# Performance work log

Measured on AMD Instinct MI355X. Metric: run time of the kernel, lower is better.

## Reference

```python
import jax, jax.numpy as jnp
import numpy as np

MODEL_DIM = 2048
N_HEADS = 16
T_MAX = 2048
LATENT = 512
DHR = 64
DK = MODEL_DIM // N_HEADS  # 128
B = 4
T = 2048


def _rope_tables(t, d):
    # pos pattern [0,0,1,1,...] matching repeat(2).reshape in source
    pos = jnp.repeat(jnp.arange(d // 2, dtype=jnp.float32), 2)
    theta = jnp.power(10000.0, -2.0 * pos / d)  # (d,)
    freq = jnp.arange(t, dtype=jnp.float32)[:, None]  # (t,1)
    ang = freq * theta[None, :]  # (t,d)
    return jnp.cos(ang), jnp.sin(ang)


def _apply_rope(x, cos, sin):
    # x: (B, nh, T, d); interleaved rotate-half: (x1,x2) -> (-x2, x1)
    b, nh, t, d = x.shape
    x2 = x.reshape(b, nh, t, d // 2, 2)
    x_rot = jnp.stack([-x2[..., 1], x2[..., 0]], axis=-1).reshape(b, nh, t, d)
    return x * cos[None, None] + x_rot * sin[None, None]


def setup_inputs() -> dict:
    key = jax.random.key(0)
    ks = jax.random.split(key, 14)
    s = 0.02
    f32 = jnp.float32
    return {
        "x": jax.random.normal(ks[0], (B, T, MODEL_DIM), dtype=f32),
        "W_down": jax.random.normal(ks[1], (MODEL_DIM, 2 * LATENT), dtype=f32) * s,
        "b_down": jnp.zeros((2 * LATENT,), dtype=f32),
        "W_uKV": jax.random.normal(ks[2], (LATENT, 2 * MODEL_DIM), dtype=f32) * s,
        "b_uKV": jnp.zeros((2 * MODEL_DIM,), dtype=f32),
        "W_uQ": jax.random.normal(ks[3], (LATENT, MODEL_DIM), dtype=f32) * s,
        "b_uQ": jnp.zeros((MODEL_DIM,), dtype=f32),
        "W_kr": jax.random.normal(ks[4], (MODEL_DIM, DHR), dtype=f32) * s,
        "b_kr": jnp.zeros((DHR,), dtype=f32),
        "W_qr": jax.random.normal(ks[5], (MODEL_DIM, DHR * N_HEADS), dtype=f32) * s,
        "b_qr": jnp.zeros((DHR * N_HEADS,), dtype=f32),
        "W_out": jax.random.normal(ks[6], (MODEL_DIM, MODEL_DIM), dtype=f32) * s,
        "b_out": jnp.zeros((MODEL_DIM,), dtype=f32),
    }


def reference(x, W_down, b_down, W_uKV, b_uKV, W_uQ, b_uQ,
              W_kr, b_kr, W_qr, b_qr, W_out, b_out):
    b, t, c = x.shape
    cos, sin = _rope_tables(T_MAX, DHR)
    cos, sin = cos[:t], sin[:t]

    # low-rank down projection -> latent for KV and latent for Q
    down = x @ W_down + b_down  # (B,T,2*LATENT)
    cKV, cq = jnp.split(down, 2, axis=-1)

    # decoupled RoPE channels
    kR = _apply_rope((x @ W_kr + b_kr)[:, None], cos, sin)  # (B,1,T,dhR)
    kR = jnp.broadcast_to(kR, (b, N_HEADS, t, DHR))
    qR = (x @ W_qr + b_qr).reshape(b, t, N_HEADS, DHR).transpose(0, 2, 1, 3)
    qR = _apply_rope(qR, cos, sin)  # (B,nh,T,dhR)

    # up-projections
    v_k = (cKV @ W_uKV + b_uKV).reshape(b, t, N_HEADS, 2 * DK).transpose(0, 2, 1, 3)
    v, k = jnp.split(v_k, 2, axis=-1)  # (B,nh,T,dk) each
    k = jnp.concatenate([k, kR], axis=-1)  # (B,nh,T,dk+dhR)
    q = (cq @ W_uQ + b_uQ).reshape(b, t, N_HEADS, DK).transpose(0, 2, 1, 3)
    q = jnp.concatenate([q, qR], axis=-1)  # (B,nh,T,dk+dhR)

    # scaled dot-product attention (unmasked, as in source; scale uses dk only)
    w = jnp.einsum('bhtd,bhsd->bhts', q, k) * (1.0 / DK ** 0.5)
    w = jax.nn.softmax(w, axis=-1)
    out = jnp.einsum('bhts,bhsd->bhtd', w, v)  # (B,nh,T,dk)
    out = out.transpose(0, 2, 1, 3).reshape(b, t, MODEL_DIM)
    return out @ W_out + b_out
```

## Files before the change

kernel.cpp:

```cpp
#include <hip/hip_runtime.h>
#include <hip/hip_bf16.h>

typedef unsigned short u16;
typedef unsigned int u32;
typedef __attribute__((ext_vector_type(4))) float f32x4;
typedef __attribute__((ext_vector_type(8))) short s16x8;

#define NHEADS 16
#define TSEQ 2048
#define BATCH 4
#define BT (BATCH*TSEQ)

__device__ __forceinline__ float bf2f(u16 v){ u32 u=((u32)v)<<16; return __builtin_bit_cast(float,u); }
__device__ __forceinline__ u16 f2bf(float f){ u32 u=__builtin_bit_cast(u32,f); u += 0x7fffu + ((u>>16)&1u); return (u16)(u>>16); }

__device__ __forceinline__ void gload16(const void* g, void* l){
  __builtin_amdgcn_global_load_lds((const __attribute__((address_space(1))) u32*)g,
                                   (__attribute__((address_space(3))) u32*)l, 16, 0, 0);
}

__global__ void cast_bf16_kernel(const float* __restrict__ in, u16* __restrict__ out, long n){
  long i = ((long)blockIdx.x*256 + threadIdx.x)*4;
  if (i >= n) return;
  float4 v = *(const float4*)(in + i);
  ushort4 o;
  o.x = f2bf(v.x); o.y = f2bf(v.y); o.z = f2bf(v.z); o.w = f2bf(v.w);
  *(ushort4*)(out + i) = o;
}

__global__ void transpose_cast_kernel(const float* __restrict__ in, u16* __restrict__ out, int R, int C){
  __shared__ float tile[32][33];
  int bc = blockIdx.x*32, br = blockIdx.y*32;
  int lx = threadIdx.x & 31, ly = threadIdx.x >> 5;
  #pragma unroll
  for (int i=0;i<32;i+=8)
    tile[ly+i][lx] = in[(long)(br+ly+i)*C + bc + lx];
  __syncthreads();
  #pragma unroll
  for (int i=0;i<32;i+=8)
    out[(long)(bc+ly+i)*R + br + lx] = f2bf(tile[lx][ly+i]);
}

__global__ void rope_tab_kernel(float* __restrict__ ctab, float* __restrict__ stab){
  int idx = blockIdx.x*256 + threadIdx.x;
  int t = idx >> 5, i = idx & 31;
  float theta = expf(-(float)i * (9.210340371976184f/32.0f));
  float ang = (float)t * theta;
  float s, c;
  sincosf(ang, &s, &c);
  ctab[idx] = c; stab[idx] = s;
}

__global__ void rope_inplace_kernel(u32* __restrict__ buf, const float* __restrict__ ct,
                                    const float* __restrict__ st, int log2ppr){
  long idx = (long)blockIdx.x*256 + threadIdx.x;
  long row = idx >> log2ppr;
  int pp = (int)(idx & ((1<<log2ppr)-1));
  int t = (int)(row & (TSEQ-1));
  int pr = pp & 31;
  u32 v = buf[idx];
  float x0 = bf2f((u16)v), x1 = bf2f((u16)(v>>16));
  float c = ct[t*32+pr], s = st[t*32+pr];
  float y0 = x0*c - x1*s;
  float y1 = x1*c + x0*s;
  buf[idx] = (u32)f2bf(y0) | ((u32)f2bf(y1)<<16);
}

template<int OUTF32>
__global__ __launch_bounds__(256,2) void gemm_bt_kernel(
    const u16* __restrict__ A, const u16* __restrict__ Bt, const float* __restrict__ bias,
    void* __restrict__ Cp, int M, int N, int K, int lda, int ldb, int ldc)
{
  __shared__ u16 As[128*32];
  __shared__ u16 Bs[128*32];
  const int tid = threadIdx.x;
  const int lane = tid & 63;
  const int wave = tid >> 6;
  const long bm = (long)blockIdx.x * 128;
  const long bn = (long)blockIdx.y * 128;
  const int wr = (wave>>1)*64, wc = (wave&1)*64;
  const int g = lane>>4, r15 = lane&15;

  f32x4 acc[4][4];
  #pragma unroll
  for (int m=0;m<4;m++)
    #pragma unroll
    for (int n=0;n<4;n++) acc[m][n] = (f32x4){0.f,0.f,0.f,0.f};

  const int c0 = tid, c1 = tid + 256;
  const u16* gA0 = A + (bm + (c0>>2))*lda + (c0&3)*8;
  const u16* gA1 = A + (bm + (c1>>2))*lda + (c1&3)*8;
  const u16* gB0 = Bt + (bn + (c0>>2))*ldb + (c0&3)*8;
  const u16* gB1 = Bt + (bn + (c1>>2))*ldb + (c1&3)*8;
  u16* lA0 = As + c0*8;
  u16* lA1 = As + c1*8;
  u16* lB0 = Bs + c0*8;
  u16* lB1 = Bs + c1*8;

  for (int k0 = 0; k0 < K; k0 += 32) {
    __syncthreads();
    gload16(gA0 + k0, lA0);
    gload16(gA1 + k0, lA1);
    gload16(gB0 + k0, lB0);
    gload16(gB1 + k0, lB1);
    __syncthreads();
    s16x8 af[4], bfr[4];
    #pragma unroll
    for (int m=0;m<4;m++) af[m] = *(const s16x8*)(As + (wr + m*16 + r15)*32 + g*8);
    #pragma unroll
    for (int n=0;n<4;n++) bfr[n] = *(const s16x8*)(Bs + (wc + n*16 + r15)*32 + g*8);
    #pragma unroll
    for (int m=0;m<4;m++)
      #pragma unroll
      for (int n=0;n<4;n++)
        acc[m][n] = __builtin_amdgcn_mfma_f32_16x16x32_bf16(af[m], bfr[n], acc[m][n], 0,0,0);
  }

  #pragma unroll
  for (int n=0;n<4;n++){
    long col = bn + wc + n*16 + r15;
    if (col >= N) continue;
    float bv = bias[col];
    #pragma unroll
    for (int m=0;m<4;m++){
      long row0 = bm + wr + m*16 + g*4;
      #pragma unroll
      for (int i=0;i<4;i++){
        long row = row0 + i;
        if (row < M){
          float v = acc[m][n][i] + bv;
          if (OUTF32) ((float*)Cp)[row*(long)ldc + col] = v;
          else        ((u16*)Cp)[row*(long)ldc + col] = f2bf(v);
        }
      }
    }
  }
}

__global__ void transpose_v_kernel(const u16* __restrict__ vk_b, u16* __restrict__ Vt){
  __shared__ u16 tile[128][130];
  int t0 = blockIdx.x*128;
  int bh = blockIdx.y;
  int b = bh>>4, h = bh&15;
  for (int idx = threadIdx.x; idx < 128*128; idx += 256){
    int r = idx>>7, c = idx&127;
    tile[r][c] = vk_b[((long)(b*TSEQ + t0 + r))*4096 + h*256 + c];
  }
  __syncthreads();
  for (int idx = threadIdx.x; idx < 128*128; idx += 256){
    int d = idx>>7, tt = idx&127;
    Vt[((long)bh*128 + d)*TSEQ + t0 + tt] = tile[tt][d];
  }
}

__global__ __launch_bounds__(256,2) void attn_kernel(
    const u16* __restrict__ q_b, const u16* __restrict__ qr_b,
    const u16* __restrict__ vk_b, const u16* __restrict__ kr_b,
    const u16* __restrict__ Vt, u16* __restrict__ attn_b)
{
  __shared__ u16 Ks[64*192];
  __shared__ u16 Vs[128*64];
  __shared__ u16 Ps[4][16*64];

  const int tid = threadIdx.x;
  const int lane = tid & 63;
  const int wave = tid >> 6;
  const int g = lane >> 4;
  const int r15 = lane & 15;
  const int bh = blockIdx.y;
  const int b = bh>>4, h = bh&15;
  const int q0 = blockIdx.x*64 + wave*16;

  s16x8 qf[6];
  {
    const u16* qp  = q_b  + ((long)b*TSEQ + q0 + r15)*2048 + h*128 + g*8;
    const u16* qrp = qr_b + ((long)b*TSEQ + q0 + r15)*1024 + h*64  + g*8;
    #pragma unroll
    for (int kd=0;kd<4;kd++) qf[kd] = *(const s16x8*)(qp + kd*32);
    #pragma unroll
    for (int kd=4;kd<6;kd++) qf[kd] = *(const s16x8*)(qrp + (kd-4)*32);
  }

  f32x4 oacc[8];
  #pragma unroll
  for (int i=0;i<8;i++) oacc[i] = (f32x4){0.f,0.f,0.f,0.f};
  float mrow[4] = {-__builtin_inff(),-__builtin_inff(),-__builtin_inff(),-__builtin_inff()};
  float lrow[4] = {0.f,0.f,0.f,0.f};

  const int krow_s = tid>>2;
  const int kslot_s = tid&3;
  const int vrow_s = tid>>1;
  const int vslot_s = tid&1;
  const u16* kbase = vk_b + (long)b*TSEQ*4096 + h*256 + 128 + kslot_s*8;
  const u16* rbase = kr_b + (long)b*TSEQ*64 + kslot_s*8;
  const long vg_base = (long)bh*128*TSEQ;
  char* KsB = (char*)Ks;
  char* VsB = (char*)Vs;
  char* PsB = (char*)(&Ps[wave][0]);

  for (int kt=0; kt<32; ++kt) {
    __syncthreads();
    {
      long t = (long)(kt*64 + krow_s);
      u32 base = (u32)((krow_s*24 + kslot_s)*16);
      u32 sw = (u32)((krow_s&7)<<4);
      #pragma unroll
      for (int j=0;j<4;j++){
        s16x8 v = *(const s16x8*)(kbase + t*4096 + j*32);
        *(s16x8*)(KsB + ((base + j*64) ^ sw)) = v;
      }
      #pragma unroll
      for (int j=4;j<6;j++){
        s16x8 v = *(const s16x8*)(rbase + t*64 + (j-4)*32);
        *(s16x8*)(KsB + ((base + j*64) ^ sw)) = v;
      }
      const u16* vsrc = Vt + vg_base + (long)vrow_s*TSEQ + kt*64 + vslot_s*8;
      u32 vbase = (u32)((vrow_s*8 + vslot_s)*16);
      u32 vsw = (u32)((vrow_s&7)<<4);
      #pragma unroll
      for (int j=0;j<4;j++){
        s16x8 v = *(const s16x8*)(vsrc + j*16);
        *(s16x8*)(VsB + ((vbase + j*32) ^ vsw)) = v;
      }
    }
    __syncthreads();

    f32x4 sacc[4];
    #pragma unroll
    for (int n=0;n<4;n++) sacc[n] = (f32x4){0.f,0.f,0.f,0.f};
    #pragma unroll
    for (int kd=0; kd<6; kd++){
      #pragma unroll
      for (int n=0;n<4;n++){
        int krow = n*16 + r15;
        u32 byt = (u32)(krow*384 + kd*64 + g*16) ^ (u32)((krow&7)<<4);
        s16x8 kfr = *(const s16x8*)(KsB + byt);
        sacc[n] = __builtin_amdgcn_mfma_f32_16x16x32_bf16(qf[kd], kfr, sacc[n], 0,0,0);
      }
    }

    const float scale = 0.08838834764831845f;
    float tmax[4];
    #pragma unroll
    for (int i=0;i<4;i++){
      float m0 = fmaxf(fmaxf(sacc[0][i],sacc[1][i]), fmaxf(sacc[2][i],sacc[3][i]));
      #pragma unroll
      for (int off=1; off<16; off<<=1) m0 = fmaxf(m0, __shfl_xor(m0, off));
      tmax[i] = m0*scale;
    }
    float psc[4];
    #pragma unroll
    for (int i=0;i<4;i++){
      float mn = fmaxf(mrow[i], tmax[i]);
      psc[i] = __expf(mrow[i]-mn);
      mrow[i] = mn;
    }
    float rs[4] = {0.f,0.f,0.f,0.f};
    #pragma unroll
    for (int n=0;n<4;n++){
      #pragma unroll
      for (int i=0;i<4;i++){
        float p = __expf(sacc[n][i]*scale - mrow[i]);
        rs[i] += p;
        int prow = g*4+i;
        u32 pb = (u32)(prow*128 + (n*16+r15)*2) ^ (u32)((prow&7)<<4);
        *(u16*)(PsB + pb) = f2bf(p);
      }
    }
    #pragma unroll
    for (int i=0;i<4;i++){
      float rsum = rs[i];
      #pragma unroll
      for (int off=1; off<16; off<<=1) rsum += __shfl_xor(rsum, off);
      lrow[i] = lrow[i]*psc[i] + rsum;
    }
    #pragma unroll
    for (int nf=0;nf<8;nf++){
      f32x4 o = oacc[nf];
      o[0]*=psc[0]; o[1]*=psc[1]; o[2]*=psc[2]; o[3]*=psc[3];
      oacc[nf] = o;
    }
    #pragma unroll
    for (int ks=0; ks<2; ks++){
      u32 pb = (u32)(r15*128 + ks*64 + g*16) ^ (u32)((r15&7)<<4);
      s16x8 pf = *(const s16x8*)(PsB + pb);
      #pragma unroll
      for (int nf=0;nf<8;nf++){
        int vrow = nf*16 + r15;
        u32 vb = (u32)(vrow*128 + ks*64 + g*16) ^ (u32)((vrow&7)<<4);
        s16x8 vf = *(const s16x8*)(VsB + vb);
        oacc[nf] = __builtin_amdgcn_mfma_f32_16x16x32_bf16(pf, vf, oacc[nf], 0,0,0);
      }
    }
  }

  #pragma unroll
  for (int nf=0;nf<8;nf++){
    #pragma unroll
    for (int i=0;i<4;i++){
      float v = oacc[nf][i] / lrow[i];
      long t = q0 + g*4 + i;
      attn_b[((long)b*TSEQ + t)*2048 + h*128 + nf*16 + r15] = f2bf(v);
    }
  }
}

extern "C" void kernel_launch(void* const* d_in, const int* in_sizes, int n_in,
                              void* d_out, int out_size, void* d_ws, size_t ws_size,
                              hipStream_t stream)
{
  const float* x      = (const float*)d_in[0];
  const float* W_down = (const float*)d_in[1];
  const float* b_down = (const float*)d_in[2];
  const float* W_uKV  = (const float*)d_in[3];
  const float* b_uKV  = (const float*)d_in[4];
  const float* W_uQ   = (const float*)d_in[5];
  const float* b_uQ   = (const float*)d_in[6];
  const float* W_kr   = (const float*)d_in[7];
  const float* b_kr   = (const float*)d_in[8];
  const float* W_qr   = (const float*)d_in[9];
  const float* b_qr   = (const float*)d_in[10];
  const float* W_out  = (const float*)d_in[11];
  const float* b_out  = (const float*)d_in[12];
  float* out = (float*)d_out;

  char* ws = (char*)d_ws;
  size_t off = 0;
  auto alloc = [&](size_t b)->char* { char* p = ws + off; off += (b + 255) & ~(size_t)255; return p; };

  u16* xb     = (u16*)alloc((size_t)BT*2048*2);
  u16* attn_b = xb;
  u16* q_b    = (u16*)alloc((size_t)BT*2048*2);
  u16* vk_b   = (u16*)alloc((size_t)BT*4096*2);
  u16* qr_b   = (u16*)alloc((size_t)BT*1024*2);
  u16* kr_b   = (u16*)alloc((size_t)BT*64*2);
  char* slot5 = alloc((size_t)64*128*TSEQ*2);
  u16* down_b = (u16*)slot5;
  u16* Vt     = (u16*)slot5;
  u16* Wd_t   = (u16*)alloc((size_t)1024*2048*2);
  u16* Wqr_t  = (u16*)alloc((size_t)1024*2048*2);
  u16* Wkr_t  = (u16*)alloc((size_t)128*2048*2);
  u16* WuKV_t = (u16*)alloc((size_t)4096*512*2);
  u16* WuQ_t  = (u16*)alloc((size_t)2048*512*2);
  u16* Wout_t = (u16*)alloc((size_t)2048*2048*2);
  float* ctab = (float*)alloc((size_t)2048*32*4);
  float* stab = (float*)alloc((size_t)2048*32*4);

  long nx = (long)BT*2048;
  cast_bf16_kernel<<<dim3((u32)(nx/4/256)), 256, 0, stream>>>(x, xb, nx);
  transpose_cast_kernel<<<dim3(32, 64), 256, 0, stream>>>(W_down, Wd_t, 2048, 1024);
  transpose_cast_kernel<<<dim3(32, 64), 256, 0, stream>>>(W_qr,  Wqr_t, 2048, 1024);
  transpose_cast_kernel<<<dim3(2, 64),  256, 0, stream>>>(W_kr,  Wkr_t, 2048, 64);
  transpose_cast_kernel<<<dim3(128,16), 256, 0, stream>>>(W_uKV, WuKV_t, 512, 4096);
  transpose_cast_kernel<<<dim3(64, 16), 256, 0, stream>>>(W_uQ,  WuQ_t, 512, 2048);
  transpose_cast_kernel<<<dim3(64, 64), 256, 0, stream>>>(W_out, Wout_t, 2048, 2048);
  rope_tab_kernel<<<dim3(256), 256, 0, stream>>>(ctab, stab);

  gemm_bt_kernel<0><<<dim3(64, 8),  256, 0, stream>>>(xb, Wd_t,  b_down, down_b, 8192, 1024, 2048, 2048, 2048, 1024);
  gemm_bt_kernel<0><<<dim3(64, 8),  256, 0, stream>>>(xb, Wqr_t, b_qr,   qr_b,   8192, 1024, 2048, 2048, 2048, 1024);
  gemm_bt_kernel<0><<<dim3(64, 1),  256, 0, stream>>>(xb, Wkr_t, b_kr,   kr_b,   8192, 64,   2048, 2048, 2048, 64);
  gemm_bt_kernel<0><<<dim3(64, 32), 256, 0, stream>>>(down_b,       WuKV_t, b_uKV, vk_b, 8192, 4096, 512, 1024, 512, 4096);
  gemm_bt_kernel<0><<<dim3(64, 16), 256, 0, stream>>>(down_b + 512, WuQ_t,  b_uQ,  q_b,  8192, 2048, 512, 1024, 512, 2048);

  rope_inplace_kernel<<<dim3(16384), 256, 0, stream>>>((u32*)qr_b, ctab, stab, 9);
  rope_inplace_kernel<<<dim3(1024),  256, 0, stream>>>((u32*)kr_b, ctab, stab, 5);
  transpose_v_kernel<<<dim3(16, 64), 256, 0, stream>>>(vk_b, Vt);

  attn_kernel<<<dim3(32, 64), 256, 0, stream>>>(q_b, qr_b, vk_b, kr_b, Vt, attn_b);

  gemm_bt_kernel<1><<<dim3(64, 16), 256, 0, stream>>>(attn_b, Wout_t, b_out, out, 8192, 2048, 2048, 2048, 2048, 2048);
}
```

Measured before the change: 927.0 us.

## Fuse input projections into one GEMM, prefetch attention tiles, add lazy rescale

Concatenates W_down, W_qr and W_kr into a single transposed weight, so the three x-projections run as one wider GEMM with a concatenated bias. The rope kernels and attention read strided slices of that buffer, and Vt now lives in the output buffer as scratch. The attention kernel prefetches the next K/V tile into registers while computing, raises wave priority around the MFMA blocks, and skips the online-softmax rescale unless the running max grows by more than 8. The lazy rescale risks fp32 overflow or precision loss, and the register prefetch raises register pressure.

```diff
diff --git a/kernel.cpp b/kernel.cpp
--- a/kernel.cpp
+++ b/kernel.cpp
@@ -51,19 +51,31 @@
   ctab[idx] = c; stab[idx] = s;
 }
 
+__global__ void concat_bias_kernel(const float* __restrict__ a, const float* __restrict__ b,
+                                   const float* __restrict__ c, float* __restrict__ o){
+  int i = blockIdx.x*256 + threadIdx.x;
+  if (i >= 2176) return;
+  float v = 0.f;
+  if (i < 1024) v = a[i];
+  else if (i < 2048) v = b[i-1024];
+  else if (i < 2112) v = c[i-2048];
+  o[i] = v;
+}
+
 __global__ void rope_inplace_kernel(u32* __restrict__ buf, const float* __restrict__ ct,
-                                    const float* __restrict__ st, int log2ppr){
+                                    const float* __restrict__ st, int log2ppr, int rstride){
   long idx = (long)blockIdx.x*256 + threadIdx.x;
   long row = idx >> log2ppr;
   int pp = (int)(idx & ((1<<log2ppr)-1));
   int t = (int)(row & (TSEQ-1));
   int pr = pp & 31;
-  u32 v = buf[idx];
+  u32* p = buf + row*(long)rstride + pp;
+  u32 v = *p;
   float x0 = bf2f((u16)v), x1 = bf2f((u16)(v>>16));
   float c = ct[t*32+pr], s = st[t*32+pr];
   float y0 = x0*c - x1*s;
   float y1 = x1*c + x0*s;
-  buf[idx] = (u32)f2bf(y0) | ((u32)f2bf(y1)<<16);
+  *p = (u32)f2bf(y0) | ((u32)f2bf(y1)<<16);
 }
 
 template<int OUTF32>
@@ -154,8 +166,8 @@
 }
 
 __global__ __launch_bounds__(256,2) void attn_kernel(
-    const u16* __restrict__ q_b, const u16* __restrict__ qr_b,
-    const u16* __restrict__ vk_b, const u16* __restrict__ kr_b,
+    const u16* __restrict__ q_b, const u16* __restrict__ qrB,
+    const u16* __restrict__ vk_b, const u16* __restrict__ krB,
     const u16* __restrict__ Vt, u16* __restrict__ attn_b)
 {
   __shared__ u16 Ks[64*192];
@@ -173,12 +185,12 @@
 
   s16x8 qf[6];
   {
-    const u16* qp  = q_b  + ((long)b*TSEQ + q0 + r15)*2048 + h*128 + g*8;
-    const u16* qrp = qr_b + ((long)b*TSEQ + q0 + r15)*1024 + h*64  + g*8;
+    const u16* qp  = q_b + ((long)b*TSEQ + q0 + r15)*2048 + h*128 + g*8;
+    const u16* qrp = qrB + ((long)b*TSEQ + q0 + r15)*2112 + h*64  + g*8;
     #pragma unroll
     for (int kd=0;kd<4;kd++) qf[kd] = *(const s16x8*)(qp + kd*32);
-    #pragma unroll
-    for (int kd=4;kd<6;kd++) qf[kd] = *(const s16x8*)(qrp + (kd-4)*32);
+    qf[4] = *(const s16x8*)(qrp);
+    qf[5] = *(const s16x8*)(qrp + 32);
   }
 
   f32x4 oacc[8];
@@ -192,42 +204,50 @@
   const int vrow_s = tid>>1;
   const int vslot_s = tid&1;
   const u16* kbase = vk_b + (long)b*TSEQ*4096 + h*256 + 128 + kslot_s*8;
-  const u16* rbase = kr_b + (long)b*TSEQ*64 + kslot_s*8;
+  const u16* rbase = krB + (long)b*TSEQ*2112 + kslot_s*8;
   const long vg_base = (long)bh*128*TSEQ;
   char* KsB = (char*)Ks;
   char* VsB = (char*)Vs;
   char* PsB = (char*)(&Ps[wave][0]);
 
+  s16x8 kreg[6], vreg[4];
+
+  auto load_regs = [&](int kt){
+    long t = (long)(kt*64 + krow_s);
+    const u16* kp = kbase + t*4096;
+    const u16* rp = rbase + t*2112;
+    #pragma unroll
+    for (int j=0;j<4;j++) kreg[j] = *(const s16x8*)(kp + j*32);
+    kreg[4] = *(const s16x8*)(rp);
+    kreg[5] = *(const s16x8*)(rp + 32);
+    const u16* vsrc = Vt + vg_base + (long)vrow_s*TSEQ + kt*64 + vslot_s*8;
+    #pragma unroll
+    for (int j=0;j<4;j++) vreg[j] = *(const s16x8*)(vsrc + j*16);
+  };
+  auto write_lds = [&](){
+    u32 base = (u32)((krow_s*24 + kslot_s)*16);
+    u32 sw = (u32)((krow_s&7)<<4);
+    #pragma unroll
+    for (int j=0;j<6;j++)
+      *(s16x8*)(KsB + ((base + j*64) ^ sw)) = kreg[j];
+    u32 vbase = (u32)((vrow_s*8 + vslot_s)*16);
+    u32 vsw = (u32)((vrow_s&7)<<4);
+    #pragma unroll
+    for (int j=0;j<4;j++)
+      *(s16x8*)(VsB + ((vbase + j*32) ^ vsw)) = vreg[j];
+  };
+
+  load_regs(0);
+  write_lds();
+  __syncthreads();
+
   for (int kt=0; kt<32; ++kt) {
-    __syncthreads();
-    {
-      long t = (long)(kt*64 + krow_s);
-      u32 base = (u32)((krow_s*24 + kslot_s)*16);
-      u32 sw = (u32)((krow_s&7)<<4);
-      #pragma unroll
-      for (int j=0;j<4;j++){
-        s16x8 v = *(const s16x8*)(kbase + t*4096 + j*32);
-        *(s16x8*)(KsB + ((base + j*64) ^ sw)) = v;
-      }
-      #pragma unroll
-      for (int j=4;j<6;j++){
-        s16x8 v = *(const s16x8*)(rbase + t*64 + (j-4)*32);
-        *(s16x8*)(KsB + ((base + j*64) ^ sw)) = v;
-      }
-      const u16* vsrc = Vt + vg_base + (long)vrow_s*TSEQ + kt*64 + vslot_s*8;
-      u32 vbase = (u32)((vrow_s*8 + vslot_s)*16);
-      u32 vsw = (u32)((vrow_s&7)<<4);
-      #pragma unroll
-      for (int j=0;j<4;j++){
-        s16x8 v = *(const s16x8*)(vsrc + j*16);
-        *(s16x8*)(VsB + ((vbase + j*32) ^ vsw)) = v;
-      }
-    }
-    __syncthreads();
+    if (kt < 31) load_regs(kt+1);
 
     f32x4 sacc[4];
     #pragma unroll
     for (int n=0;n<4;n++) sacc[n] = (f32x4){0.f,0.f,0.f,0.f};
+    __builtin_amdgcn_s_setprio(1);
     #pragma unroll
     for (int kd=0; kd<6; kd++){
       #pragma unroll
@@ -238,6 +258,7 @@
         sacc[n] = __builtin_amdgcn_mfma_f32_16x16x32_bf16(qf[kd], kfr, sacc[n], 0,0,0);
       }
     }
+    __builtin_amdgcn_s_setprio(0);
 
     const float scale = 0.08838834764831845f;
     float tmax[4];
@@ -248,12 +269,24 @@
       for (int off=1; off<16; off<<=1) m0 = fmaxf(m0, __shfl_xor(m0, off));
       tmax[i] = m0*scale;
     }
-    float psc[4];
-    #pragma unroll
-    for (int i=0;i<4;i++){
-      float mn = fmaxf(mrow[i], tmax[i]);
-      psc[i] = __expf(mrow[i]-mn);
-      mrow[i] = mn;
+    float grow = 0.f;
+    #pragma unroll
+    for (int i=0;i<4;i++) grow = fmaxf(grow, tmax[i]-mrow[i]);
+    if (__any(grow > 8.0f)){
+      float psc[4];
+      #pragma unroll
+      for (int i=0;i<4;i++){
+        float mn = fmaxf(mrow[i], tmax[i]);
+        psc[i] = __expf(mrow[i]-mn);
+        mrow[i] = mn;
+        lrow[i] *= psc[i];
+      }
+      #pragma unroll
+      for (int nf=0;nf<8;nf++){
+        f32x4 o = oacc[nf];
+        o[0]*=psc[0]; o[1]*=psc[1]; o[2]*=psc[2]; o[3]*=psc[3];
+        oacc[nf] = o;
+      }
     }
     float rs[4] = {0.f,0.f,0.f,0.f};
     #pragma unroll
@@ -272,14 +305,10 @@
       float rsum = rs[i];
       #pragma unroll
       for (int off=1; off<16; off<<=1) rsum += __shfl_xor(rsum, off);
-      lrow[i] = lrow[i]*psc[i] + rsum;
-    }
-    #pragma unroll
-    for (int nf=0;nf<8;nf++){
-      f32x4 o = oacc[nf];
-      o[0]*=psc[0]; o[1]*=psc[1]; o[2]*=psc[2]; o[3]*=psc[3];
-      oacc[nf] = o;
-    }
+      lrow[i] += rsum;
+    }
+
+    __builtin_amdgcn_s_setprio(1);
     #pragma unroll
     for (int ks=0; ks<2; ks++){
       u32 pb = (u32)(r15*128 + ks*64 + g*16) ^ (u32)((r15&7)<<4);
@@ -292,6 +321,11 @@
         oacc[nf] = __builtin_amdgcn_mfma_f32_16x16x32_bf16(pf, vf, oacc[nf], 0,0,0);
       }
     }
+    __builtin_amdgcn_s_setprio(0);
+
+    __syncthreads();
+    if (kt < 31) write_lds();
+    __syncthreads();
   }
 
   #pragma unroll
@@ -332,41 +366,36 @@
   u16* attn_b = xb;
   u16* q_b    = (u16*)alloc((size_t)BT*2048*2);
   u16* vk_b   = (u16*)alloc((size_t)BT*4096*2);
-  u16* qr_b   = (u16*)alloc((size_t)BT*1024*2);
-  u16* kr_b   = (u16*)alloc((size_t)BT*64*2);
-  char* slot5 = alloc((size_t)64*128*TSEQ*2);
-  u16* down_b = (u16*)slot5;
-  u16* Vt     = (u16*)slot5;
-  u16* Wd_t   = (u16*)alloc((size_t)1024*2048*2);
-  u16* Wqr_t  = (u16*)alloc((size_t)1024*2048*2);
-  u16* Wkr_t  = (u16*)alloc((size_t)128*2048*2);
+  u16* C1     = (u16*)alloc((size_t)BT*2112*2);
+  u16* W1_t   = (u16*)alloc((size_t)2176*2048*2);
   u16* WuKV_t = (u16*)alloc((size_t)4096*512*2);
   u16* WuQ_t  = (u16*)alloc((size_t)2048*512*2);
   u16* Wout_t = (u16*)alloc((size_t)2048*2048*2);
   float* ctab = (float*)alloc((size_t)2048*32*4);
   float* stab = (float*)alloc((size_t)2048*32*4);
+  float* bias1= (float*)alloc((size_t)2176*4);
+  u16* Vt     = (u16*)d_out;
 
   long nx = (long)BT*2048;
   cast_bf16_kernel<<<dim3((u32)(nx/4/256)), 256, 0, stream>>>(x, xb, nx);
-  transpose_cast_kernel<<<dim3(32, 64), 256, 0, stream>>>(W_down, Wd_t, 2048, 1024);
-  transpose_cast_kernel<<<dim3(32, 64), 256, 0, stream>>>(W_qr,  Wqr_t, 2048, 1024);
-  transpose_cast_kernel<<<dim3(2, 64),  256, 0, stream>>>(W_kr,  Wkr_t, 2048, 64);
+  transpose_cast_kernel<<<dim3(32, 64), 256, 0, stream>>>(W_down, W1_t,             2048, 1024);
+  transpose_cast_kernel<<<dim3(32, 64), 256, 0, stream>>>(W_qr,  W1_t + 1024*2048,  2048, 1024);
+  transpose_cast_kernel<<<dim3(2, 64),  256, 0, stream>>>(W_kr,  W1_t + 2048*2048,  2048, 64);
   transpose_cast_kernel<<<dim3(128,16), 256, 0, stream>>>(W_uKV, WuKV_t, 512, 4096);
   transpose_cast_kernel<<<dim3(64, 16), 256, 0, stream>>>(W_uQ,  WuQ_t, 512, 2048);
   transpose_cast_kernel<<<dim3(64, 64), 256, 0, stream>>>(W_out, Wout_t, 2048, 2048);
   rope_tab_kernel<<<dim3(256), 256, 0, stream>>>(ctab, stab);
-
-  gemm_bt_kernel<0><<<dim3(64, 8),  256, 0, stream>>>(xb, Wd_t,  b_down, down_b, 8192, 1024, 2048, 2048, 2048, 1024);
-  gemm_bt_kernel<0><<<dim3(64, 8),  256, 0, stream>>>(xb, Wqr_t, b_qr,   qr_b,   8192, 1024, 2048, 2048, 2048, 1024);
-  gemm_bt_kernel<0><<<dim3(64, 1),  256, 0, stream>>>(xb, Wkr_t, b_kr,   kr_b,   8192, 64,   2048, 2048, 2048, 64);
-  gemm_bt_kernel<0><<<dim3(64, 32), 256, 0, stream>>>(down_b,       WuKV_t, b_uKV, vk_b, 8192, 4096, 512, 1024, 512, 4096);
-  gemm_bt_kernel<0><<<dim3(64, 16), 256, 0, stream>>>(down_b + 512, WuQ_t,  b_uQ,  q_b,  8192, 2048, 512, 1024, 512, 2048);
-
-  rope_inplace_kernel<<<dim3(16384), 256, 0, stream>>>((u32*)qr_b, ctab, stab, 9);
-  rope_inplace_kernel<<<dim3(1024),  256, 0, stream>>>((u32*)kr_b, ctab, stab, 5);
+  concat_bias_kernel<<<dim3(9), 256, 0, stream>>>(b_down, b_qr, b_kr, bias1);
+
+  gemm_bt_kernel<0><<<dim3(64, 17), 256, 0, stream>>>(xb, W1_t, bias1, C1, 8192, 2112, 2048, 2048, 2048, 2112);
+  gemm_bt_kernel<0><<<dim3(64, 32), 256, 0, stream>>>(C1,       WuKV_t, b_uKV, vk_b, 8192, 4096, 512, 2112, 512, 4096);
+  gemm_bt_kernel<0><<<dim3(64, 16), 256, 0, stream>>>(C1 + 512, WuQ_t,  b_uQ,  q_b,  8192, 2048, 512, 2112, 512, 2048);
+
+  rope_inplace_kernel<<<dim3(16384), 256, 0, stream>>>((u32*)(C1 + 1024), ctab, stab, 9, 1056);
+  rope_inplace_kernel<<<dim3(1024),  256, 0, stream>>>((u32*)(C1 + 2048), ctab, stab, 5, 1056);
   transpose_v_kernel<<<dim3(16, 64), 256, 0, stream>>>(vk_b, Vt);
 
-  attn_kernel<<<dim3(32, 64), 256, 0, stream>>>(q_b, qr_b, vk_b, kr_b, Vt, attn_b);
+  attn_kernel<<<dim3(32, 64), 256, 0, stream>>>(q_b, C1 + 1024, vk_b, C1 + 2048, Vt, attn_b);
 
   gemm_bt_kernel<1><<<dim3(64, 16), 256, 0, stream>>>(attn_b, Wout_t, b_out, out, 8192, 2048, 2048, 2048, 2048, 2048);
 }
```

Measured after the change: 900.7 us. -2.8%, faster.
